# Kernel tuning notes

Measured on AMD Instinct MI355X. Metric: run time of the kernel, lower is better.

## Reference

```python
import jax, jax.numpy as jnp
import numpy as np

B, T = 256, 128
IN_DIMS = [300, 100, 512]
HID = [128, 64, 128]
FC = [100, 50, 100]
DH, DF, NC = 256, 128, 6  # dialogue hidden / dialogue fc / n_classes


def _uniform(k, shape, bound):
    return jax.random.uniform(k, shape, jnp.float32, -bound, bound)


def setup_inputs() -> dict:
    key = jax.random.key(0)
    ks = iter(jax.random.split(key, 64))
    d = {}
    for i, dim in enumerate(IN_DIMS):
        d[f"mod{i}"] = jax.random.normal(next(ks), (B, T, dim), jnp.float32)
    d["umask"] = jnp.ones((B, T), jnp.float32)
    # per-modality LSTMCell + FC params (torch init: U(-1/sqrt(H), 1/sqrt(H)))
    for i, (din, h, f) in enumerate(zip(IN_DIMS, HID, FC)):
        s = 1.0 / np.sqrt(h)
        d[f"w_ih{i}"] = _uniform(next(ks), (4 * h, din), s)
        d[f"w_hh{i}"] = _uniform(next(ks), (4 * h, h), s)
        d[f"b_ih{i}"] = _uniform(next(ks), (4 * h,), s)
        d[f"b_hh{i}"] = _uniform(next(ks), (4 * h,), s)
        sf = 1.0 / np.sqrt(h)
        d[f"fc_w{i}"] = _uniform(next(ks), (f, h), sf)
        d[f"fc_b{i}"] = _uniform(next(ks), (f,), sf)
    # dialogue-level LSTMCell + output heads
    sumfc = sum(FC)
    sd = 1.0 / np.sqrt(DH)
    d["w_ih_d"] = _uniform(next(ks), (4 * DH, sumfc), sd)
    d["w_hh_d"] = _uniform(next(ks), (4 * DH, DH), sd)
    d["b_ih_d"] = _uniform(next(ks), (4 * DH,), sd)
    d["b_hh_d"] = _uniform(next(ks), (4 * DH,), sd)
    d["fc_out_w"] = _uniform(next(ks), (DF, DH), sd)
    d["fc_out_b"] = _uniform(next(ks), (DF,), sd)
    sm = 1.0 / np.sqrt(DF)
    d["smax_w"] = _uniform(next(ks), (NC, DF), sm)
    d["smax_b"] = _uniform(next(ks), (NC,), sm)
    return d


def _lstm_step(h, c, xt, w_ih, w_hh, b):
    # torch LSTMCell gate order: i, f, g, o
    g = xt @ w_ih.T + h @ w_hh.T + b
    i_, f_, g_, o_ = jnp.split(g, 4, axis=-1)
    c2 = jax.nn.sigmoid(f_) * c + jax.nn.sigmoid(i_) * jnp.tanh(g_)
    h2 = jax.nn.sigmoid(o_) * jnp.tanh(c2)
    return h2, c2


def reference(mod0, mod1, mod2, umask,
              w_ih0, w_hh0, b_ih0, b_hh0, fc_w0, fc_b0,
              w_ih1, w_hh1, b_ih1, b_hh1, fc_w1, fc_b1,
              w_ih2, w_hh2, b_ih2, b_hh2, fc_w2, fc_b2,
              w_ih_d, w_hh_d, b_ih_d, b_hh_d,
              fc_out_w, fc_out_b, smax_w, smax_b):
    b = mod0.shape[0]
    umask_t = jnp.swapaxes(umask, 0, 1)[:, :, None]  # [T, B, 1]
    mods = [mod0, mod1, mod2]
    params = [(w_ih0, w_hh0, b_ih0 + b_hh0, fc_w0, fc_b0),
              (w_ih1, w_hh1, b_ih1 + b_hh1, fc_w1, fc_b1),
              (w_ih2, w_hh2, b_ih2 + b_hh2, fc_w2, fc_b2)]
    feats = []
    for mod, (wi, wh, bb, fw, fb) in zip(mods, params):
        H = wh.shape[1]
        xs = jnp.swapaxes(mod, 0, 1) * umask_t  # [T, B, D]

        def step(carry, xt, wi=wi, wh=wh, bb=bb, fw=fw, fb=fb):
            h, c = carry
            h2, c2 = _lstm_step(h, c, xt, wi, wh, bb)
            h2 = jnp.tanh(h2)  # extra tanh on hidden state (dropout = identity in eval)
            return (h2, c2), jnp.tanh(h2 @ fw.T + fb)

        init = (jnp.zeros((b, H), mod.dtype), jnp.zeros((b, H), mod.dtype))
        _, ys = jax.lax.scan(step, init, xs)  # ys: [T, B, fc]
        feats.append(ys)

    dfeat = jnp.concatenate(feats, axis=-1) * umask_t  # [T, B, sum(fc)]
    bd = b_ih_d + b_hh_d

    def dstep(carry, xt):
        h, c = carry
        h2, c2 = _lstm_step(h, c, xt, w_ih_d, w_hh_d, bd)
        return (h2, c2), jnp.tanh(h2 @ fc_out_w.T + fc_out_b)

    dh = w_hh_d.shape[1]
    init = (jnp.zeros((b, dh), dfeat.dtype), jnp.zeros((b, dh), dfeat.dtype))
    _, hs = jax.lax.scan(dstep, init, dfeat)  # [T, B, DF]
    logits = hs @ smax_w.T + smax_b           # [T, B, NC]
    out = jnp.swapaxes(logits, 0, 1)          # [B, T, NC]
    return jax.nn.log_softmax(out, axis=2)
```

## Files before the change

kernel.cpp:

```cpp
#include <hip/hip_runtime.h>

#define B_ 256
#define T_ 128
#define M_ (B_ * T_)
#define DH_ 256

__device__ __forceinline__ float sigf(float x) { return 1.0f / (1.0f + __expf(-x)); }
__device__ __forceinline__ float dot4(float4 a, float4 b) {
  return a.x * b.x + a.y * b.y + a.z * b.z + a.w * b.w;
}

typedef _Float16 half2v __attribute__((ext_vector_type(2)));
typedef short short8 __attribute__((ext_vector_type(8)));
typedef float f32x4 __attribute__((ext_vector_type(4)));

__device__ __forceinline__ float fdot2f(unsigned int w, unsigned int h, float acc) {
  half2v wv = __builtin_bit_cast(half2v, w);
  half2v hv = __builtin_bit_cast(half2v, h);
#if __has_builtin(__builtin_amdgcn_fdot2)
  return __builtin_amdgcn_fdot2(wv, hv, acc, false);
#else
  return acc + (float)wv[0] * (float)hv[0] + (float)wv[1] * (float)hv[1];
#endif
}
__device__ __forceinline__ unsigned int pk16(float a, float b) {
  unsigned short lo = __builtin_bit_cast(unsigned short, (_Float16)a);
  unsigned short hi = __builtin_bit_cast(unsigned short, (_Float16)b);
  return (unsigned int)lo | ((unsigned int)hi << 16);
}
__device__ __forceinline__ unsigned short bf16c(float x) {
  unsigned int u = __builtin_bit_cast(unsigned int, x);
  return (unsigned short)((u + 0x7FFFu + ((u >> 16) & 1u)) >> 16);
}
__device__ __forceinline__ unsigned int bfpk(float a, float b) {
  return (unsigned int)bf16c(a) | ((unsigned int)bf16c(b) << 16);
}

__global__ void prep_kernel(const float* __restrict__ w_ih_d, const float* __restrict__ w_hh_d,
                            const float* __restrict__ b_ih_d, const float* __restrict__ b_hh_d,
                            const float* __restrict__ b_ih0, const float* __restrict__ b_hh0,
                            const float* __restrict__ b_ih1, const float* __restrict__ b_hh1,
                            const float* __restrict__ b_ih2, const float* __restrict__ b_hh2,
                            const float* __restrict__ w_hh0, const float* __restrict__ w_hh1,
                            const float* __restrict__ w_hh2,
                            const float* __restrict__ w_ih0, const float* __restrict__ w_ih1,
                            const float* __restrict__ w_ih2,
                            const float* __restrict__ fc_w0, const float* __restrict__ fc_w1,
                            const float* __restrict__ fc_w2,
                            unsigned short* __restrict__ dfeat_h,
                            float* __restrict__ biasd, float* __restrict__ bias0,
                            float* __restrict__ bias1, float* __restrict__ bias2,
                            unsigned int* __restrict__ wpk, unsigned int* __restrict__ wldsg,
                            unsigned int* __restrict__ wpk0, unsigned int* __restrict__ wpk1,
                            unsigned int* __restrict__ wpk2,
                            unsigned short* __restrict__ w0b, unsigned short* __restrict__ w1b,
                            unsigned short* __restrict__ w2b, unsigned short* __restrict__ wdb,
                            unsigned short* __restrict__ fcw0b, unsigned short* __restrict__ fcw1b,
                            unsigned short* __restrict__ fcw2b) {
  int idx = blockIdx.x * blockDim.x + threadIdx.x;
  int stride = gridDim.x * blockDim.x;
  for (int i = idx; i < 512 * 320; i += stride) {
    int r = i / 320, k = i % 320;
    w0b[i] = (k < 300) ? bf16c(w_ih0[(size_t)r * 300 + k]) : (unsigned short)0;
  }
  for (int i = idx; i < 256 * 128; i += stride) {
    int r = i >> 7, k = i & 127;
    w1b[i] = (k < 100) ? bf16c(w_ih1[(size_t)r * 100 + k]) : (unsigned short)0;
  }
  for (int i = idx; i < 512 * 512; i += stride) w2b[i] = bf16c(w_ih2[i]);
  for (int i = idx; i < 1024 * 256; i += stride) {
    int r = i >> 8, k = i & 255;
    wdb[i] = (k < 250) ? bf16c(w_ih_d[(size_t)r * 250 + k]) : (unsigned short)0;
  }
  for (int i = idx; i < 128 * 128; i += stride) {
    int f = i >> 7, k = i & 127;
    fcw0b[i] = (f < 100) ? bf16c(fc_w0[(size_t)f * 128 + k]) : (unsigned short)0;
    fcw2b[i] = (f < 100) ? bf16c(fc_w2[(size_t)f * 128 + k]) : (unsigned short)0;
  }
  for (int i = idx; i < 64 * 64; i += stride) {
    int f = i >> 6, k = i & 63;
    fcw1b[i] = (f < 50) ? bf16c(fc_w1[(size_t)f * 64 + k]) : (unsigned short)0;
  }
  for (int i = idx; i < M_ * 6; i += stride)
    dfeat_h[(size_t)(i / 6) * 256 + 250 + (i % 6)] = 0;
  for (int i = idx; i < 1024 * 96; i += stride) {
    int r = i / 96, k0 = (i % 96) * 2;
    wpk[i] = pk16(w_hh_d[(size_t)r * 256 + k0], w_hh_d[(size_t)r * 256 + k0 + 1]);
  }
  for (int i = idx; i < 32768; i += stride) {
    int jj = i >> 12, rem = i & 4095, r = rem >> 2, q = rem & 3;
    int p = 96 + 4 * jj + q;
    wldsg[i] = pk16(w_hh_d[(size_t)r * 256 + 2 * p], w_hh_d[(size_t)r * 256 + 2 * p + 1]);
  }
  for (int i = idx; i < 512 * 64; i += stride) {
    int r = i >> 6, p = (i & 63) * 2;
    wpk0[i] = pk16(w_hh0[(size_t)r * 128 + p], w_hh0[(size_t)r * 128 + p + 1]);
    wpk2[i] = pk16(w_hh2[(size_t)r * 128 + p], w_hh2[(size_t)r * 128 + p + 1]);
  }
  for (int i = idx; i < 256 * 32; i += stride) {
    int r = i >> 5, p = (i & 31) * 2;
    wpk1[i] = pk16(w_hh1[(size_t)r * 64 + p], w_hh1[(size_t)r * 64 + p + 1]);
  }
  for (int i = idx; i < 1024; i += stride) biasd[i] = b_ih_d[i] + b_hh_d[i];
  for (int i = idx; i < 512; i += stride) bias0[i] = b_ih0[i] + b_hh0[i];
  for (int i = idx; i < 256; i += stride) bias1[i] = b_ih1[i] + b_hh1[i];
  for (int i = idx; i < 512; i += stride) bias2[i] = b_ih2[i] + b_hh2[i];
}

template <bool XF16>
__global__ __launch_bounds__(256) void mfma_gemm(
    const void* __restrict__ Xv, const unsigned short* __restrict__ Wb,
    const float* __restrict__ bias, const float* __restrict__ umask,
    float* __restrict__ C, int K, int Kp, int N) {
  __shared__ __align__(16) unsigned short Xs[64][40];
  __shared__ __align__(16) unsigned short Ws[64][40];
  const int tid = threadIdx.x;
  const int d = blockIdx.x;
  const int nx = N >> 6;
  const int n0 = ((d % (nx << 3)) >> 3) << 6;
  const int m0 = (((d / (nx << 3)) << 3) + (d & 7)) << 6;
  const int srow = tid >> 2, kq = tid & 3;
  const int w = tid >> 6, lane = tid & 63;
  const int lr = lane & 15, lk = lane >> 4;
  const float* Xf = nullptr;
  const unsigned short* Xh = nullptr;
  if constexpr (XF16) {
    Xh = (const unsigned short*)Xv + (size_t)(m0 + srow) * Kp;
  } else {
    const int t = m0 >> 8, b0 = m0 & 255;
    Xf = (const float*)Xv + ((size_t)(b0 + srow) * T_ + t) * K;
  }
  const unsigned short* Wr = Wb + (size_t)(n0 + srow) * Kp;
  f32x4 acc[4];
#pragma unroll
  for (int j = 0; j < 4; j++) acc[j] = (f32x4){0.f, 0.f, 0.f, 0.f};

  for (int k0 = 0; k0 < Kp; k0 += 32) {
    uint4 xa;
    const int kk = k0 + kq * 8;
    if constexpr (XF16) {
      xa = *reinterpret_cast<const uint4*>(Xh + kk);
    } else {
      float4 va = (kk + 3 < K) ? *reinterpret_cast<const float4*>(Xf + kk)
                               : make_float4(0.f, 0.f, 0.f, 0.f);
      float4 vb = (kk + 7 < K) ? *reinterpret_cast<const float4*>(Xf + kk + 4)
                               : make_float4(0.f, 0.f, 0.f, 0.f);
      xa.x = bfpk(va.x, va.y); xa.y = bfpk(va.z, va.w);
      xa.z = bfpk(vb.x, vb.y); xa.w = bfpk(vb.z, vb.w);
    }
    uint4 wv = *reinterpret_cast<const uint4*>(Wr + kk);
    __syncthreads();
    *reinterpret_cast<uint4*>(&Xs[srow][kq * 8]) = xa;
    *reinterpret_cast<uint4*>(&Ws[srow][kq * 8]) = wv;
    __syncthreads();
    short8 af = *reinterpret_cast<const short8*>(&Xs[w * 16 + lr][lk * 8]);
#pragma unroll
    for (int j = 0; j < 4; j++) {
      short8 bf = *reinterpret_cast<const short8*>(&Ws[j * 16 + lr][lk * 8]);
      acc[j] = __builtin_amdgcn_mfma_f32_16x16x32_bf16(af, bf, acc[j], 0, 0, 0);
    }
  }
#pragma unroll
  for (int j = 0; j < 4; j++) {
    const int col = n0 + j * 16 + lr;
    const float bv = bias[col];
#pragma unroll
    for (int r = 0; r < 4; r++) {
      const int mrow = m0 + w * 16 + lk * 4 + r;
      float um = 1.0f;
      if constexpr (!XF16)
        um = umask[((m0 & 255) + w * 16 + lk * 4 + r) * T_ + (m0 >> 8)];
      C[(size_t)mrow * N + col] = acc[j][r] * um + bv;
    }
  }
}

__global__ __launch_bounds__(256) void fc_gemm(
    const unsigned short* __restrict__ Xh, const unsigned short* __restrict__ Wb,
    const float* __restrict__ fcb, const float* __restrict__ umask,
    unsigned short* __restrict__ dfeat_h, int Kp, int nx, int F, int col0) {
  __shared__ __align__(16) unsigned short Xs[64][40];
  __shared__ __align__(16) unsigned short Ws[64][40];
  const int tid = threadIdx.x;
  const int n0 = (blockIdx.x % nx) * 64;
  const int m0 = (blockIdx.x / nx) * 64;
  const int srow = tid >> 2, kq = tid & 3;
  const int w = tid >> 6, lane = tid & 63;
  const int lr = lane & 15, lk = lane >> 4;
  const unsigned short* Xp = Xh + (size_t)(m0 + srow) * Kp;
  const unsigned short* Wr = Wb + (size_t)(n0 + srow) * Kp;
  f32x4 acc[4];
#pragma unroll
  for (int j = 0; j < 4; j++) acc[j] = (f32x4){0.f, 0.f, 0.f, 0.f};
  for (int k0 = 0; k0 < Kp; k0 += 32) {
    const int kk = k0 + kq * 8;
    uint4 xa = *reinterpret_cast<const uint4*>(Xp + kk);
    uint4 wv = *reinterpret_cast<const uint4*>(Wr + kk);
    __syncthreads();
    *reinterpret_cast<uint4*>(&Xs[srow][kq * 8]) = xa;
    *reinterpret_cast<uint4*>(&Ws[srow][kq * 8]) = wv;
    __syncthreads();
    short8 af = *reinterpret_cast<const short8*>(&Xs[w * 16 + lr][lk * 8]);
#pragma unroll
    for (int j = 0; j < 4; j++) {
      short8 bf = *reinterpret_cast<const short8*>(&Ws[j * 16 + lr][lk * 8]);
      acc[j] = __builtin_amdgcn_mfma_f32_16x16x32_bf16(af, bf, acc[j], 0, 0, 0);
    }
  }
#pragma unroll
  for (int j = 0; j < 4; j++) {
    const int coln = n0 + j * 16 + lr;
    const float bv = (coln < F) ? fcb[coln] : 0.f;
#pragma unroll
    for (int r = 0; r < 4; r++) {
      const int mrow = m0 + w * 16 + lk * 4 + r;
      if (coln < F) {
        const int t = mrow >> 8, b = mrow & 255;
        float um = umask[b * T_ + t];
        dfeat_h[(size_t)mrow * 256 + col0 + coln] = bf16c(tanhf(acc[j][r] + bv) * um);
      }
    }
  }
}

struct ModScanArgs {
  const float* gx0; const float* gx1; const float* gx2;
  const unsigned int* wk0; const unsigned int* wk1; const unsigned int* wk2;
  unsigned short* hm0; unsigned short* hm1; unsigned short* hm2;
};

__device__ __forceinline__ void mod_body128s(
    const float* __restrict__ gx, const unsigned int* __restrict__ wk,
    int b, unsigned short* __restrict__ hallm, unsigned int* smem) {
  float* gbuf = (float*)smem;
  unsigned int* hbuf = smem + 512;
  const int tid = threadIdx.x;
  uint4 wrA[16], wrB[16];
  {
    const uint4* wpA = reinterpret_cast<const uint4*>(wk + (size_t)tid * 64);
    const uint4* wpB = reinterpret_cast<const uint4*>(wk + (size_t)(tid + 256) * 64);
#pragma unroll
    for (int j = 0; j < 16; j++) { wrA[j] = wpA[j]; wrB[j] = wpB[j]; }
  }
  if (tid < 64) hbuf[tid] = 0u;
  float creg = 0.f;
  __syncthreads();
  const uint4* h4 = reinterpret_cast<const uint4*>(hbuf);
  const float* gp = gx + (size_t)b * 512 + tid;
  float gcA = gp[0], gcB = gp[256];
  for (int t = 0; t < T_; t++) {
    float gnA = 0.f, gnB = 0.f;
    if (t + 1 < T_) {
      gnA = gp[(size_t)(t + 1) * B_ * 512];
      gnB = gp[(size_t)(t + 1) * B_ * 512 + 256];
    }
    float a0 = 0.f, a1 = 0.f, a2 = 0.f, a3 = 0.f;
    float d0 = 0.f, d1 = 0.f, d2 = 0.f, d3 = 0.f;
#pragma unroll
    for (int j = 0; j < 16; j++) {
      uint4 hv = h4[j];
      a0 = fdot2f(wrA[j].x, hv.x, a0);
      a1 = fdot2f(wrA[j].y, hv.y, a1);
      a2 = fdot2f(wrA[j].z, hv.z, a2);
      a3 = fdot2f(wrA[j].w, hv.w, a3);
      d0 = fdot2f(wrB[j].x, hv.x, d0);
      d1 = fdot2f(wrB[j].y, hv.y, d1);
      d2 = fdot2f(wrB[j].z, hv.z, d2);
      d3 = fdot2f(wrB[j].w, hv.w, d3);
    }
    gbuf[tid] = (a0 + a1) + (a2 + a3) + gcA;
    gbuf[tid + 256] = (d0 + d1) + (d2 + d3) + gcB;
    gcA = gnA; gcB = gnB;
    __syncthreads();
    if (tid < 128) {
      float i_ = sigf(gbuf[tid]);
      float f_ = sigf(gbuf[128 + tid]);
      float g_ = tanhf(gbuf[256 + tid]);
      float o_ = sigf(gbuf[384 + tid]);
      float cc = f_ * creg + i_ * g_;
      creg = cc;
      float h2 = tanhf(o_ * tanhf(cc));
      hallm[((size_t)t * B_ + b) * 128 + tid] = bf16c(h2);
      float hp = __shfl_xor(h2, 1);
      if ((tid & 1) == 0) hbuf[tid >> 1] = pk16(h2, hp);
    }
    __syncthreads();
  }
}

__device__ __forceinline__ void mod_body64s(
    const float* __restrict__ gx, const unsigned int* __restrict__ wk,
    int b, unsigned short* __restrict__ hallm, unsigned int* smem) {
  float* gbuf = (float*)smem;
  unsigned int* hbuf = smem + 512;
  const int tid = threadIdx.x;
  uint4 wr[8];
  {
    const uint4* wp = reinterpret_cast<const uint4*>(wk + (size_t)tid * 32);
#pragma unroll
    for (int j = 0; j < 8; j++) wr[j] = wp[j];
  }
  if (tid < 32) hbuf[tid] = 0u;
  float creg = 0.f;
  __syncthreads();
  const uint4* h4 = reinterpret_cast<const uint4*>(hbuf);
  const float* gp = gx + (size_t)b * 256 + tid;
  float gc = gp[0];
  for (int t = 0; t < T_; t++) {
    float gn = (t + 1 < T_) ? gp[(size_t)(t + 1) * B_ * 256] : 0.f;
    float a0 = 0.f, a1 = 0.f, a2 = 0.f, a3 = 0.f;
#pragma unroll
    for (int j = 0; j < 8; j++) {
      uint4 hv = h4[j];
      a0 = fdot2f(wr[j].x, hv.x, a0);
      a1 = fdot2f(wr[j].y, hv.y, a1);
      a2 = fdot2f(wr[j].z, hv.z, a2);
      a3 = fdot2f(wr[j].w, hv.w, a3);
    }
    gbuf[tid] = (a0 + a1) + (a2 + a3) + gc;
    gc = gn;
    __syncthreads();
    if (tid < 64) {
      float i_ = sigf(gbuf[tid]);
      float f_ = sigf(gbuf[64 + tid]);
      float g_ = tanhf(gbuf[128 + tid]);
      float o_ = sigf(gbuf[192 + tid]);
      float cc = f_ * creg + i_ * g_;
      creg = cc;
      float h2 = tanhf(o_ * tanhf(cc));
      hallm[((size_t)t * B_ + b) * 64 + tid] = bf16c(h2);
      float hp = __shfl_xor(h2, 1);
      if ((tid & 1) == 0) hbuf[tid >> 1] = pk16(h2, hp);
    }
    __syncthreads();
  }
}

__global__ __launch_bounds__(256)
__attribute__((amdgpu_waves_per_eu(2, 3)))
void mod_scan(ModScanArgs a, unsigned short* __restrict__ hm_unused) {
  __shared__ __align__(16) unsigned int smem[576];
  const int blk = blockIdx.x;
  if (blk < 512) {
    const int mi = blk >> 8, b = blk & 255;
    mod_body128s(mi ? a.gx2 : a.gx0, mi ? a.wk2 : a.wk0, b,
                 mi ? a.hm2 : a.hm0, smem);
  } else {
    mod_body64s(a.gx1, a.wk1, blk - 512, a.hm1, smem);
  }
}

#define DLG_LDS_BYTES (131072 + 4096 + 512)

__global__ __launch_bounds__(512, 2) void dlg_recur(
    const float* __restrict__ gxd, const unsigned int* __restrict__ wpk,
    const unsigned int* __restrict__ wldsg, float* __restrict__ hall) {
  extern __shared__ char smem[];
  unsigned int* wl = (unsigned int*)smem;
  float* gbuf = (float*)(smem + 131072);
  _Float16* hbuf_h = (_Float16*)(smem + 131072 + 4096);
  const uint4* hbuf4 = (const uint4*)hbuf_h;
  const uint4* wl4 = (const uint4*)wl;
  const int tid = threadIdx.x;
  const int b = blockIdx.x;

  for (int i = tid; i < 32768; i += 512) wl[i] = wldsg[i];
  unsigned int wr0[96], wr1[96];
  {
    const uint4* p0 = reinterpret_cast<const uint4*>(wpk + (size_t)tid * 96);
    const uint4* p1 = reinterpret_cast<const uint4*>(wpk + (size_t)(tid + 512) * 96);
#pragma unroll
    for (int j = 0; j < 24; j++) {
      uint4 v0 = p0[j], v1 = p1[j];
      wr0[4 * j + 0] = v0.x; wr0[4 * j + 1] = v0.y; wr0[4 * j + 2] = v0.z; wr0[4 * j + 3] = v0.w;
      wr1[4 * j + 0] = v1.x; wr1[4 * j + 1] = v1.y; wr1[4 * j + 2] = v1.z; wr1[4 * j + 3] = v1.w;
    }
  }
  if (tid < 32) reinterpret_cast<uint4*>(const_cast<_Float16*>(hbuf_h))[tid] = uint4{0, 0, 0, 0};
  float creg = 0.f;
  __syncthreads();

  const float* gbase = gxd + (size_t)b * 1024 + tid;
  float gc0 = gbase[0], gc1 = gbase[512];
  for (int t = 0; t < T_; t++) {
    float gn0 = 0.f, gn1 = 0.f;
    if (t + 1 < T_) {
      gn0 = gbase[(size_t)(t + 1) * B_ * 1024];
      gn1 = gbase[(size_t)(t + 1) * B_ * 1024 + 512];
    }
    float a0 = 0.f, a1 = 0.f;
#pragma unroll
    for (int j = 0; j < 24; j++) {
      uint4 hv = hbuf4[j];
      a0 = fdot2f(wr0[4 * j + 0], hv.x, a0); a1 = fdot2f(wr1[4 * j + 0], hv.x, a1);
      a0 = fdot2f(wr0[4 * j + 1], hv.y, a0); a1 = fdot2f(wr1[4 * j + 1], hv.y, a1);
      a0 = fdot2f(wr0[4 * j + 2], hv.z, a0); a1 = fdot2f(wr1[4 * j + 2], hv.z, a1);
      a0 = fdot2f(wr0[4 * j + 3], hv.w, a0); a1 = fdot2f(wr1[4 * j + 3], hv.w, a1);
    }
#pragma unroll
    for (int jj = 0; jj < 8; jj++) {
      uint4 hv = hbuf4[24 + jj];
      uint4 wa = wl4[jj * 1024 + tid];
      uint4 wc = wl4[jj * 1024 + tid + 512];
      a0 = fdot2f(wa.x, hv.x, a0); a1 = fdot2f(wc.x, hv.x, a1);
      a0 = fdot2f(wa.y, hv.y, a0); a1 = fdot2f(wc.y, hv.y, a1);
      a0 = fdot2f(wa.z, hv.z, a0); a1 = fdot2f(wc.z, hv.z, a1);
      a0 = fdot2f(wa.w, hv.w, a0); a1 = fdot2f(wc.w, hv.w, a1);
    }
    gbuf[tid] = a0 + gc0;
    gbuf[tid + 512] = a1 + gc1;
    __syncthreads();
    if (tid < DH_) {
      float i_ = sigf(gbuf[tid]);
      float f_ = sigf(gbuf[DH_ + tid]);
      float g_ = tanhf(gbuf[2 * DH_ + tid]);
      float o_ = sigf(gbuf[3 * DH_ + tid]);
      float c2 = f_ * creg + i_ * g_;
      creg = c2;
      float h2 = o_ * tanhf(c2);
      hall[((size_t)t * B_ + b) * DH_ + tid] = h2;
      hbuf_h[tid] = (_Float16)h2;
    }
    gc0 = gn0; gc1 = gn1;
    __syncthreads();
  }
}

__global__ __launch_bounds__(256) void out_head(
    const float* __restrict__ hall, const float* __restrict__ fcow,
    const float* __restrict__ fcob, const float* __restrict__ smw,
    const float* __restrict__ smb, float* __restrict__ out) {
  __shared__ __align__(16) float h_lds[16][260];
  __shared__ __align__(16) float fco[16][132];
  __shared__ float lg[16][6];
  const int tid = threadIdx.x;
  const int m0 = blockIdx.x * 16;
  {
    const float* src = hall + (size_t)m0 * DH_;
    for (int e = tid; e < 1024; e += 256) {
      float4 v = reinterpret_cast<const float4*>(src)[e];
      const int r = e >> 6, k = (e & 63) * 4;
      *reinterpret_cast<float4*>(&h_lds[r][k]) = v;
    }
  }
  __syncthreads();
  {
    const int f = tid & 127, half = tid >> 7;
    float acc[8];
    const float fb = fcob[f];
#pragma unroll
    for (int r = 0; r < 8; r++) acc[r] = fb;
    const float* wrow = fcow + (size_t)f * DH_;
    for (int k = 0; k < DH_; k += 4) {
      float4 w4 = *reinterpret_cast<const float4*>(wrow + k);
#pragma unroll
      for (int r = 0; r < 8; r++)
        acc[r] += dot4(w4, *reinterpret_cast<const float4*>(&h_lds[half * 8 + r][k]));
    }
#pragma unroll
    for (int r = 0; r < 8; r++) fco[half * 8 + r][f] = tanhf(acc[r]);
  }
  __syncthreads();
  if (tid < 96) {
    const int r = tid / 6, cc = tid % 6;
    float a = smb[cc];
    const float* sw = smw + cc * 128;
#pragma unroll 4
    for (int k = 0; k < 128; k++) a += sw[k] * fco[r][k];
    lg[r][cc] = a;
  }
  __syncthreads();
  if (tid < 16) {
    const int m = m0 + tid;
    const int t = m >> 8, b = m & 255;
    float mx = lg[tid][0];
#pragma unroll
    for (int cc = 1; cc < 6; cc++) mx = fmaxf(mx, lg[tid][cc]);
    float ssum = 0.f;
#pragma unroll
    for (int cc = 0; cc < 6; cc++) ssum += __expf(lg[tid][cc] - mx);
    float lse = mx + logf(ssum);
#pragma unroll
    for (int cc = 0; cc < 6; cc++)
      out[((size_t)b * T_ + t) * 6 + cc] = lg[tid][cc] - lse;
  }
}

extern "C" void kernel_launch(void* const* d_in, const int* in_sizes, int n_in,
                              void* d_out, int out_size, void* d_ws, size_t ws_size,
                              hipStream_t stream) {
  const float* mod0  = (const float*)d_in[0];
  const float* mod1  = (const float*)d_in[1];
  const float* mod2  = (const float*)d_in[2];
  const float* umask = (const float*)d_in[3];
  const float* w_ih0 = (const float*)d_in[4];
  const float* w_hh0 = (const float*)d_in[5];
  const float* b_ih0 = (const float*)d_in[6];
  const float* b_hh0 = (const float*)d_in[7];
  const float* fc_w0 = (const float*)d_in[8];
  const float* fc_b0 = (const float*)d_in[9];
  const float* w_ih1 = (const float*)d_in[10];
  const float* w_hh1 = (const float*)d_in[11];
  const float* b_ih1 = (const float*)d_in[12];
  const float* b_hh1 = (const float*)d_in[13];
  const float* fc_w1 = (const float*)d_in[14];
  const float* fc_b1 = (const float*)d_in[15];
  const float* w_ih2 = (const float*)d_in[16];
  const float* w_hh2 = (const float*)d_in[17];
  const float* b_ih2 = (const float*)d_in[18];
  const float* b_hh2 = (const float*)d_in[19];
  const float* fc_w2 = (const float*)d_in[20];
  const float* fc_b2 = (const float*)d_in[21];
  const float* w_ih_d = (const float*)d_in[22];
  const float* w_hh_d = (const float*)d_in[23];
  const float* b_ih_d = (const float*)d_in[24];
  const float* b_hh_d = (const float*)d_in[25];
  const float* fco_w  = (const float*)d_in[26];
  const float* fco_b  = (const float*)d_in[27];
  const float* sm_w   = (const float*)d_in[28];
  const float* sm_b   = (const float*)d_in[29];

  float* ws    = (float*)d_ws;
  float* gx0   = ws;
  float* gx1   = gx0 + (size_t)M_ * 512;
  float* gx2   = gx1 + (size_t)M_ * 256;
  float* gxd   = ws;
  float* hall  = ws + (size_t)M_ * 1024;
  unsigned short* hm0 = (unsigned short*)(ws + (size_t)M_ * 1024);
  unsigned short* hm2 = hm0 + (size_t)M_ * 128;
  unsigned short* hm1 = hm2 + (size_t)M_ * 128;
  unsigned short* dfeat_h = (unsigned short*)(ws + (size_t)M_ * 1280);
  float* tail  = ws + (size_t)M_ * 1408;
  float* biasd = tail;
  float* bias0 = biasd + 1024;
  float* bias1 = bias0 + 512;
  float* bias2 = bias1 + 256;
  unsigned int* wpk   = (unsigned int*)(bias2 + 512);
  unsigned int* wldsg = wpk + 1024 * 96;
  unsigned int* wpk0  = wldsg + 32768;
  unsigned int* wpk1  = wpk0 + 512 * 64;
  unsigned int* wpk2  = wpk1 + 256 * 32;
  unsigned short* w0b = (unsigned short*)(wpk2 + 512 * 64);
  unsigned short* w1b = w0b + 512 * 320;
  unsigned short* w2b = w1b + 256 * 128;
  unsigned short* wdb = w2b + 512 * 512;
  unsigned short* fcw0b = wdb + 1024 * 256;
  unsigned short* fcw1b = fcw0b + 128 * 128;
  unsigned short* fcw2b = fcw1b + 64 * 64;

  prep_kernel<<<256, 256, 0, stream>>>(w_ih_d, w_hh_d, b_ih_d, b_hh_d,
      b_ih0, b_hh0, b_ih1, b_hh1, b_ih2, b_hh2,
      w_hh0, w_hh1, w_hh2, w_ih0, w_ih1, w_ih2, fc_w0, fc_w1, fc_w2,
      dfeat_h, biasd, bias0, bias1, bias2, wpk, wldsg,
      wpk0, wpk1, wpk2, w0b, w1b, w2b, wdb, fcw0b, fcw1b, fcw2b);

  mfma_gemm<false><<<8 * 512, 256, 0, stream>>>(mod0, w0b, bias0, umask, gx0, 300, 320, 512);
  mfma_gemm<false><<<4 * 512, 256, 0, stream>>>(mod1, w1b, bias1, umask, gx1, 100, 128, 256);
  mfma_gemm<false><<<8 * 512, 256, 0, stream>>>(mod2, w2b, bias2, umask, gx2, 512, 512, 512);

  ModScanArgs a;
  a.gx0 = gx0; a.gx1 = gx1; a.gx2 = gx2;
  a.wk0 = wpk0; a.wk1 = wpk1; a.wk2 = wpk2;
  a.hm0 = hm0; a.hm1 = hm1; a.hm2 = hm2;
  mod_scan<<<768, 256, 0, stream>>>(a, nullptr);

  fc_gemm<<<512 * 2, 256, 0, stream>>>(hm0, fcw0b, fc_b0, umask, dfeat_h, 128, 2, 100, 0);
  fc_gemm<<<512 * 1, 256, 0, stream>>>(hm1, fcw1b, fc_b1, umask, dfeat_h, 64, 1, 50, 100);
  fc_gemm<<<512 * 2, 256, 0, stream>>>(hm2, fcw2b, fc_b2, umask, dfeat_h, 128, 2, 100, 150);

  mfma_gemm<true><<<16 * 512, 256, 0, stream>>>(dfeat_h, wdb, biasd, nullptr, gxd, 256, 256, 1024);

  hipFuncSetAttribute(reinterpret_cast<const void*>(dlg_recur),
                      hipFuncAttributeMaxDynamicSharedMemorySize, DLG_LDS_BYTES);
  dlg_recur<<<256, 512, DLG_LDS_BYTES, stream>>>(gxd, wpk, wldsg, hall);

  out_head<<<M_ / 16, 256, 0, stream>>>(hall, fco_w, fco_b, sm_w, sm_b, (float*)d_out);
}
```

Before: 729.4 us.

## Use 1024 threads per dialogue LSTM block, one gate row per thread

The dialogue recurrence kernel now launches 1024 threads per batch element, and each thread computes one gate row instead of two. Per-thread register weights drop from 192 to 96 words, and the dot product is split over four independent accumulators to shorten the dependency chains. The risk is higher barrier cost and more waves competing for the CU. The launch bound changes from (512, 2) to 1024, and the register budget and occupancy change with it.

Measured after the change: 929.4 us. +27.4%, slower.

```diff
diff --git a/kernel.cpp b/kernel.cpp
--- a/kernel.cpp
+++ b/kernel.cpp
@@ -352,7 +352,7 @@
 
 #define DLG_LDS_BYTES (131072 + 4096 + 512)
 
-__global__ __launch_bounds__(512, 2) void dlg_recur(
+__global__ __launch_bounds__(1024) void dlg_recur(
     const float* __restrict__ gxd, const unsigned int* __restrict__ wpk,
     const unsigned int* __restrict__ wldsg, float* __restrict__ hall) {
   extern __shared__ char smem[];
@@ -364,16 +364,15 @@
   const int tid = threadIdx.x;
   const int b = blockIdx.x;
 
-  for (int i = tid; i < 32768; i += 512) wl[i] = wldsg[i];
-  unsigned int wr0[96], wr1[96];
+  for (int i = tid; i < 32768; i += 1024) wl[i] = wldsg[i];
+  unsigned int wr[96];
   {
     const uint4* p0 = reinterpret_cast<const uint4*>(wpk + (size_t)tid * 96);
-    const uint4* p1 = reinterpret_cast<const uint4*>(wpk + (size_t)(tid + 512) * 96);
 #pragma unroll
     for (int j = 0; j < 24; j++) {
-      uint4 v0 = p0[j], v1 = p1[j];
-      wr0[4 * j + 0] = v0.x; wr0[4 * j + 1] = v0.y; wr0[4 * j + 2] = v0.z; wr0[4 * j + 3] = v0.w;
-      wr1[4 * j + 0] = v1.x; wr1[4 * j + 1] = v1.y; wr1[4 * j + 2] = v1.z; wr1[4 * j + 3] = v1.w;
+      uint4 v0 = p0[j];
+      wr[4 * j + 0] = v0.x; wr[4 * j + 1] = v0.y;
+      wr[4 * j + 2] = v0.z; wr[4 * j + 3] = v0.w;
     }
   }
   if (tid < 32) reinterpret_cast<uint4*>(const_cast<_Float16*>(hbuf_h))[tid] = uint4{0, 0, 0, 0};
@@ -381,34 +380,29 @@
   __syncthreads();
 
   const float* gbase = gxd + (size_t)b * 1024 + tid;
-  float gc0 = gbase[0], gc1 = gbase[512];
+  float gc = gbase[0];
   for (int t = 0; t < T_; t++) {
-    float gn0 = 0.f, gn1 = 0.f;
-    if (t + 1 < T_) {
-      gn0 = gbase[(size_t)(t + 1) * B_ * 1024];
-      gn1 = gbase[(size_t)(t + 1) * B_ * 1024 + 512];
-    }
-    float a0 = 0.f, a1 = 0.f;
+    float gn = (t + 1 < T_) ? gbase[(size_t)(t + 1) * B_ * 1024] : 0.f;
+    float a0 = 0.f, a1 = 0.f, a2 = 0.f, a3 = 0.f;
 #pragma unroll
     for (int j = 0; j < 24; j++) {
       uint4 hv = hbuf4[j];
-      a0 = fdot2f(wr0[4 * j + 0], hv.x, a0); a1 = fdot2f(wr1[4 * j + 0], hv.x, a1);
-      a0 = fdot2f(wr0[4 * j + 1], hv.y, a0); a1 = fdot2f(wr1[4 * j + 1], hv.y, a1);
-      a0 = fdot2f(wr0[4 * j + 2], hv.z, a0); a1 = fdot2f(wr1[4 * j + 2], hv.z, a1);
-      a0 = fdot2f(wr0[4 * j + 3], hv.w, a0); a1 = fdot2f(wr1[4 * j + 3], hv.w, a1);
+      a0 = fdot2f(wr[4 * j + 0], hv.x, a0);
+      a1 = fdot2f(wr[4 * j + 1], hv.y, a1);
+      a2 = fdot2f(wr[4 * j + 2], hv.z, a2);
+      a3 = fdot2f(wr[4 * j + 3], hv.w, a3);
     }
 #pragma unroll
     for (int jj = 0; jj < 8; jj++) {
       uint4 hv = hbuf4[24 + jj];
       uint4 wa = wl4[jj * 1024 + tid];
-      uint4 wc = wl4[jj * 1024 + tid + 512];
-      a0 = fdot2f(wa.x, hv.x, a0); a1 = fdot2f(wc.x, hv.x, a1);
-      a0 = fdot2f(wa.y, hv.y, a0); a1 = fdot2f(wc.y, hv.y, a1);
-      a0 = fdot2f(wa.z, hv.z, a0); a1 = fdot2f(wc.z, hv.z, a1);
-      a0 = fdot2f(wa.w, hv.w, a0); a1 = fdot2f(wc.w, hv.w, a1);
-    }
-    gbuf[tid] = a0 + gc0;
-    gbuf[tid + 512] = a1 + gc1;
+      a0 = fdot2f(wa.x, hv.x, a0);
+      a1 = fdot2f(wa.y, hv.y, a1);
+      a2 = fdot2f(wa.z, hv.z, a2);
+      a3 = fdot2f(wa.w, hv.w, a3);
+    }
+    gbuf[tid] = (a0 + a1) + (a2 + a3) + gc;
+    gc = gn;
     __syncthreads();
     if (tid < DH_) {
       float i_ = sigf(gbuf[tid]);
@@ -421,7 +415,6 @@
       hall[((size_t)t * B_ + b) * DH_ + tid] = h2;
       hbuf_h[tid] = (_Float16)h2;
     }
-    gc0 = gn0; gc1 = gn1;
     __syncthreads();
   }
 }
@@ -572,7 +565,7 @@
 
   hipFuncSetAttribute(reinterpret_cast<const void*>(dlg_recur),
                       hipFuncAttributeMaxDynamicSharedMemorySize, DLG_LDS_BYTES);
-  dlg_recur<<<256, 512, DLG_LDS_BYTES, stream>>>(gxd, wpk, wldsg, hall);
+  dlg_recur<<<256, 1024, DLG_LDS_BYTES, stream>>>(gxd, wpk, wldsg, hall);
 
   out_head<<<M_ / 16, 256, 0, stream>>>(hall, fco_w, fco_b, sm_w, sm_b, (float*)d_out);
 }
```
